# Kernel tuning notes

Measured on AMD Instinct MI355X. Metric: run time of the kernel, lower is better.

Reference implementation:

```python
import jax, jax.numpy as jnp
import numpy as np

S = 1024   # speakers_per_batch
U = 64     # utterances_per_speaker
E = 256    # model_embedding_size


def setup_inputs() -> dict:
    key = jax.random.key(0)
    k1, _ = jax.random.split(key)
    # embeds as produced by forward(): relu'd then L2-normalized rows
    raw = jax.nn.relu(jax.random.normal(k1, (S * U, E), dtype=jnp.float32))
    embeds = raw / (jnp.linalg.norm(raw, axis=1, keepdims=True) + 1e-12)
    return {
        "embeds": embeds,
        "similarity_weight": jnp.array([10.0], dtype=jnp.float32),
        "similarity_bias": jnp.array([-5.0], dtype=jnp.float32),
    }


def reference(embeds, similarity_weight, similarity_bias):
    e = embeds.reshape(S, U, E)                      # [S,U,E]
    # inclusive centroids (per speaker)
    c_incl = jnp.mean(e, axis=1)                     # [S,E]
    incl_norm = jnp.linalg.norm(c_incl, axis=1)      # [S]
    # exclusive centroids (leave-one-out per utterance)
    c_excl = (jnp.sum(e, axis=1, keepdims=True) - e) / (U - 1)  # [S,U,E]
    excl_norm = jnp.linalg.norm(c_excl, axis=2)      # [S,U]
    # off-diagonal (k != j): cosine vs inclusive centroid of speaker k
    sim = jnp.einsum('jue,ke->juk', e, c_incl) / incl_norm       # [S,U,S]
    # diagonal (k == j): cosine vs own exclusive centroid
    diag = jnp.einsum('jue,jue->ju', e, c_excl) / excl_norm      # [S,U]
    idx = jnp.arange(S)
    sim = sim.at[idx, :, idx].set(diag)
    sim = sim * similarity_weight[0] + similarity_bias[0]
    # cross-entropy against ground truth speaker ids
    logits = sim.reshape(S * U, S)                   # [SU,S]
    gt = jnp.repeat(jnp.arange(S), U)                # [SU]
    logp = jax.nn.log_softmax(logits, axis=-1)
    loss = -jnp.mean(jnp.take_along_axis(logp, gt[:, None], axis=1))
    preds = jnp.argmax(logits, axis=1)
    accuracy = jnp.mean((preds == gt).astype(jnp.float32))
    return loss, accuracy
```

## Files before the change

kernel.cpp:

```cpp
#include <hip/hip_runtime.h>
#include <math.h>

#define NS 1024
#define NU 64
#define NE 256

typedef __attribute__((ext_vector_type(4))) float f32x4;
typedef long i64x2 __attribute__((ext_vector_type(2)));

__device__ static inline unsigned int pk4_fp8(float a, float b, float c,
                                              float d) {
  int r = 0;
  r = __builtin_amdgcn_cvt_pk_fp8_f32(a, b, r, false);
  r = __builtin_amdgcn_cvt_pk_fp8_f32(c, d, r, true);
  return (unsigned int)r;
}


__global__ __launch_bounds__(256) void centroid_kernel(
    const float* __restrict__ embeds, unsigned int* __restrict__ Cb,
    unsigned long long* __restrict__ Ab, float* __restrict__ normsum,
    float* __restrict__ ssumG, unsigned int* __restrict__ pmaxG,
    float* __restrict__ out) {
  int k = blockIdx.x;
  int t = threadIdx.x;
  if (t < 64) {
    ssumG[k * 64 + t] = 0.f;
    pmaxG[k * 64 + t] = 0u;
  }
  int wave = t >> 6, e4 = t & 63;

  const float4* base =
      (const float4*)(embeds + (size_t)k * NU * NE) + wave * 16 * 64 + e4;
  float4 s = {0.f, 0.f, 0.f, 0.f};
#pragma unroll
  for (int i = 0; i < 16; ++i) {
    float4 v = base[i * 64];
    s.x += v.x; s.y += v.y; s.z += v.z; s.w += v.w;
  }
  __shared__ float4 ps[4][64];
  ps[wave][e4] = s;
  __syncthreads();
  if (t < 64) {
    float4 a = ps[0][t], b = ps[1][t], c = ps[2][t], d = ps[3][t];
    float4 s4;
    s4.x = a.x + b.x + c.x + d.x;
    s4.y = a.y + b.y + c.y + d.y;
    s4.z = a.z + b.z + c.z + d.z;
    s4.w = a.w + b.w + c.w + d.w;
    float sq = s4.x * s4.x + s4.y * s4.y + s4.z * s4.z + s4.w * s4.w;
#pragma unroll
    for (int off = 32; off; off >>= 1) sq += __shfl_xor(sq, off, 64);
    float nrm = sqrtf(sq);
    float inv = 1.f / nrm;
    unsigned int v = pk4_fp8(s4.x * inv, s4.y * inv, s4.z * inv, s4.w * inv);
    int lane_ = (((t >> 1) & 3) * 16 + (k & 15));
    int idx = (k >> 4) * 1024 + (t >> 4) * 256 + lane_ * 4 +
              (((t >> 3) & 1) << 1) + (t & 1);
    Cb[idx] = v;
    if (t == 0) {
      normsum[k] = nrm;
      if (k == 0) { out[0] = 0.f; out[1] = 0.f; }
    }
  }

  {
    int tile = t >> 6;
    int l = t & 63;
    int m = l & 15, qq = l >> 4;
    const float* rowp = embeds + (size_t)(k * 64 + tile * 16 + m) * NE;
    i64x2* Ab2 = (i64x2*)Ab;
    size_t base2 = ((size_t)k * 4 + tile) * 256 + l;
#pragma unroll
    for (int s2 = 0; s2 < 4; ++s2) {
      unsigned long long u[2];
#pragma unroll
      for (int half = 0; half < 2; ++half) {
        int sI = 2 * s2 + half;
        int k0 = sI * 32 + qq * 8;
        float4 x = *(const float4*)(rowp + k0);
        float4 y = *(const float4*)(rowp + k0 + 4);
        unsigned int lo = pk4_fp8(x.x, x.y, x.z, x.w);
        unsigned int hi = pk4_fp8(y.x, y.y, y.z, y.w);
        u[half] = ((unsigned long long)hi << 32) | lo;
      }
      i64x2 v;
      v.x = (long)u[0];
      v.y = (long)u[1];
      Ab2[base2 + s2 * 64] = v;
    }
  }
}

__global__ __launch_bounds__(256, 4) void main_kernel(
    const long* __restrict__ Ab, const long* __restrict__ Cb,
    const float* __restrict__ normsum, const float* __restrict__ wp,
    const float* __restrict__ bp, float* __restrict__ ssumG,
    unsigned int* __restrict__ pmaxG, float* __restrict__ pdiagG) {
  int t = threadIdx.x;
  int wave = t >> 6, lane = t & 63;
  int c = lane & 15, q = lane >> 4;
  int b = blockIdx.x;
  int rg = b >> 1;
  int h = b & 1;
  int jspk = rg * 2 + (wave >> 1);
  int r0 = rg * 128 + wave * 32;

  float w = *wp, bia = *bp;
  const float L2E = 1.4426950408889634f;
  float M0 = fabsf(w) + bia;
  float wl = w * L2E;
  float cl = (bia - M0) * L2E;
  float ns = normsum[jspk];

  const i64x2* Av = (const i64x2*)Ab;
  const i64x2* Bv = (const i64x2*)Cb;

  long af[2][8];
#pragma unroll
  for (int mt = 0; mt < 2; ++mt) {
    int ab2 = ((r0 >> 4) + mt) * 256 + lane;
#pragma unroll
    for (int s2 = 0; s2 < 4; ++s2) {
      i64x2 v = Av[ab2 + s2 * 64];
      af[mt][2 * s2] = v.x;
      af[mt][2 * s2 + 1] = v.y;
    }
  }

  float ssum[2][4];
  float pm[2][4];
#pragma unroll
  for (int mt = 0; mt < 2; ++mt)
#pragma unroll
    for (int r = 0; r < 4; ++r) {
      ssum[mt][r] = 0.f;
      pm[mt][r] = 0.f;
    }

  auto prefetch = [&](i64x2 (&BF)[4], int Tt) {
    int cb = (h * 32 + Tt) * 256 + lane;
#pragma unroll
    for (int s2 = 0; s2 < 4; ++s2) BF[s2] = Bv[cb + s2 * 64];
  };

  auto tile = [&](f32x4 (&ACC)[2], const i64x2 (&BF)[4]) {
    ACC[0] = (f32x4){0.f, 0.f, 0.f, 0.f};
    ACC[1] = (f32x4){0.f, 0.f, 0.f, 0.f};
    __builtin_amdgcn_s_setprio(1);
#pragma unroll
    for (int s2 = 0; s2 < 4; ++s2) {
      ACC[0] = __builtin_amdgcn_mfma_f32_16x16x32_fp8_fp8(af[0][2 * s2],
                                                          BF[s2].x, ACC[0], 0, 0, 0);
      ACC[1] = __builtin_amdgcn_mfma_f32_16x16x32_fp8_fp8(af[1][2 * s2],
                                                          BF[s2].x, ACC[1], 0, 0, 0);
      ACC[0] = __builtin_amdgcn_mfma_f32_16x16x32_fp8_fp8(af[0][2 * s2 + 1],
                                                          BF[s2].y, ACC[0], 0, 0, 0);
      ACC[1] = __builtin_amdgcn_mfma_f32_16x16x32_fp8_fp8(af[1][2 * s2 + 1],
                                                          BF[s2].y, ACC[1], 0, 0, 0);
    }
    __builtin_amdgcn_s_setprio(0);
  };

  auto epilogue = [&](f32x4 (&ACC)[2], int Tt) {
    int gt = h * 32 + Tt;
    bool diagstep = ((jspk >> 4) == gt);
#pragma unroll
    for (int mt = 0; mt < 2; ++mt) {
      f32x4 a = ACC[mt];
      if (diagstep && c == (jspk & 15)) {
#pragma unroll
        for (int r = 0; r < 4; ++r) {
          float Sv = a[r] * ns;
          float den = fmaxf(fmaf(ns, ns, 1.f) - 2.f * Sv, 1e-30f);
          float val = (Sv - 1.f) * __frsqrt_rn(den);
          float pd = exp2f(fmaf(val, wl, cl));
          pdiagG[r0 + mt * 16 + q * 4 + r] = pd;
          a[r] = val;
        }
      }
#pragma unroll
      for (int r = 0; r < 4; ++r) {
        float p = exp2f(fmaf(a[r], wl, cl));
        ssum[mt][r] += p;
        pm[mt][r] = fmaxf(pm[mt][r], p);
      }
    }
  };

  i64x2 bf0[4], bf1[4];
  f32x4 accA[2], accB[2];
  prefetch(bf0, 0);
  prefetch(bf1, 1);
  tile(accA, bf0);
#pragma unroll 1
  for (int T = 1; T < 31; T += 2) {
    prefetch(bf0, T + 1);
    tile(accB, bf1);
    epilogue(accA, T - 1);
    prefetch(bf1, T + 2);
    tile(accA, bf0);
    epilogue(accB, T);
  }
  tile(accB, bf1);
  epilogue(accA, 30);
  epilogue(accB, 31);

#pragma unroll
  for (int mt = 0; mt < 2; ++mt)
#pragma unroll
    for (int r = 0; r < 4; ++r) {
      float s = ssum[mt][r];
      s += __shfl_xor(s, 1, 64);
      s += __shfl_xor(s, 2, 64);
      s += __shfl_xor(s, 4, 64);
      s += __shfl_xor(s, 8, 64);
      float m = pm[mt][r];
      m = fmaxf(m, __shfl_xor(m, 1, 64));
      m = fmaxf(m, __shfl_xor(m, 2, 64));
      m = fmaxf(m, __shfl_xor(m, 4, 64));
      m = fmaxf(m, __shfl_xor(m, 8, 64));
      if (c == 0) {
        int row = r0 + mt * 16 + q * 4 + r;
        atomicAdd(&ssumG[row], s);
        atomicMax(&pmaxG[row], __float_as_uint(m));
      }
    }
}

__global__ __launch_bounds__(256) void reduce_kernel(
    const float* __restrict__ ssumG, const unsigned int* __restrict__ pmaxG,
    const float* __restrict__ pdiagG, float* __restrict__ out) {
  int i = blockIdx.x * 256 + threadIdx.x;
  float pd = pdiagG[i];
  float lossr = __logf(ssumG[i] / pd);
  float corr = (pd >= __uint_as_float(pmaxG[i])) ? 1.f : 0.f;
#pragma unroll
  for (int off = 32; off; off >>= 1) {
    lossr += __shfl_xor(lossr, off, 64);
    corr += __shfl_xor(corr, off, 64);
  }
  __shared__ float pl[4], pc[4];
  int wave = threadIdx.x >> 6, lane = threadIdx.x & 63;
  if (lane == 0) { pl[wave] = lossr; pc[wave] = corr; }
  __syncthreads();
  if (threadIdx.x == 0) {
    const float inv = 1.f / (float)(NS * NU);
    atomicAdd(&out[0], (pl[0] + pl[1] + pl[2] + pl[3]) * inv);
    atomicAdd(&out[1], (pc[0] + pc[1] + pc[2] + pc[3]) * inv);
  }
}

extern "C" void kernel_launch(void* const* d_in, const int* in_sizes, int n_in,
                              void* d_out, int out_size, void* d_ws,
                              size_t ws_size, hipStream_t stream) {
  const float* embeds = (const float*)d_in[0];
  const float* w = (const float*)d_in[1];
  const float* b = (const float*)d_in[2];
  float* out = (float*)d_out;
  char* ws = (char*)d_ws;
  unsigned int* Cb = (unsigned int*)ws;
  unsigned int* pmaxG = (unsigned int*)(ws + (256 << 10));
  float* ssumG = (float*)(ws + (512 << 10));
  float* pdiagG = (float*)(ws + (768 << 10));
  float* normsum = (float*)(ws + (1024 << 10));
  unsigned long long* Ab =
      (unsigned long long*)(ws + (1056 << 10));

  centroid_kernel<<<NS, 256, 0, stream>>>(embeds, Cb, Ab, normsum, ssumG,
                                          pmaxG, out);
  main_kernel<<<1024, 256, 0, stream>>>((const long*)Ab, (const long*)Cb,
                                        normsum, w, b, ssumG, pmaxG, pdiagG);
  reduce_kernel<<<NS * NU / 256, 256, 0, stream>>>(ssumG, pmaxG, pdiagG, out);
}
```

Before: 145.1 us.

## Halve per-wave row tile and split K across two accumulators to double grid

Each wave now handles 16 rows instead of 32, with the 256-deep K reduction split into two independent MFMA accumulator chains that are summed in the epilogue. The grid doubles to 2048 blocks and launch bounds target 8 blocks per SM to raise occupancy. The aim is better latency hiding and lower register pressure. The cost is that every B tile is now loaded twice as often per output row, doubling centroid traffic, and more atomics are issued.

```diff
diff --git a/kernel.cpp b/kernel.cpp
--- a/kernel.cpp
+++ b/kernel.cpp
@@ -92,7 +92,7 @@
   }
 }
 
-__global__ __launch_bounds__(256, 4) void main_kernel(
+__global__ __launch_bounds__(256, 8) void main_kernel(
     const long* __restrict__ Ab, const long* __restrict__ Cb,
     const float* __restrict__ normsum, const float* __restrict__ wp,
     const float* __restrict__ bp, float* __restrict__ ssumG,
@@ -103,8 +103,8 @@
   int b = blockIdx.x;
   int rg = b >> 1;
   int h = b & 1;
-  int jspk = rg * 2 + (wave >> 1);
-  int r0 = rg * 128 + wave * 32;
+  int jspk = rg;
+  int r0 = rg * 64 + wave * 16;
 
   float w = *wp, bia = *bp;
   const float L2E = 1.4426950408889634f;
@@ -116,27 +116,23 @@
   const i64x2* Av = (const i64x2*)Ab;
   const i64x2* Bv = (const i64x2*)Cb;
 
-  long af[2][8];
-#pragma unroll
-  for (int mt = 0; mt < 2; ++mt) {
-    int ab2 = ((r0 >> 4) + mt) * 256 + lane;
+  long af[8];
+  {
+    int ab2 = (rg * 4 + wave) * 256 + lane;
 #pragma unroll
     for (int s2 = 0; s2 < 4; ++s2) {
       i64x2 v = Av[ab2 + s2 * 64];
-      af[mt][2 * s2] = v.x;
-      af[mt][2 * s2 + 1] = v.y;
-    }
-  }
-
-  float ssum[2][4];
-  float pm[2][4];
-#pragma unroll
-  for (int mt = 0; mt < 2; ++mt)
-#pragma unroll
-    for (int r = 0; r < 4; ++r) {
-      ssum[mt][r] = 0.f;
-      pm[mt][r] = 0.f;
-    }
+      af[2 * s2] = v.x;
+      af[2 * s2 + 1] = v.y;
+    }
+  }
+
+  float ssum[4], pm[4];
+#pragma unroll
+  for (int r = 0; r < 4; ++r) {
+    ssum[r] = 0.f;
+    pm[r] = 0.f;
+  }
 
   auto prefetch = [&](i64x2 (&BF)[4], int Tt) {
     int cb = (h * 32 + Tt) * 256 + lane;
@@ -149,15 +145,15 @@
     ACC[1] = (f32x4){0.f, 0.f, 0.f, 0.f};
     __builtin_amdgcn_s_setprio(1);
 #pragma unroll
-    for (int s2 = 0; s2 < 4; ++s2) {
-      ACC[0] = __builtin_amdgcn_mfma_f32_16x16x32_fp8_fp8(af[0][2 * s2],
-                                                          BF[s2].x, ACC[0], 0, 0, 0);
-      ACC[1] = __builtin_amdgcn_mfma_f32_16x16x32_fp8_fp8(af[1][2 * s2],
-                                                          BF[s2].x, ACC[1], 0, 0, 0);
-      ACC[0] = __builtin_amdgcn_mfma_f32_16x16x32_fp8_fp8(af[0][2 * s2 + 1],
-                                                          BF[s2].y, ACC[0], 0, 0, 0);
-      ACC[1] = __builtin_amdgcn_mfma_f32_16x16x32_fp8_fp8(af[1][2 * s2 + 1],
-                                                          BF[s2].y, ACC[1], 0, 0, 0);
+    for (int s2 = 0; s2 < 2; ++s2) {
+      ACC[0] = __builtin_amdgcn_mfma_f32_16x16x32_fp8_fp8(
+          af[2 * s2], BF[s2].x, ACC[0], 0, 0, 0);
+      ACC[1] = __builtin_amdgcn_mfma_f32_16x16x32_fp8_fp8(
+          af[2 * s2 + 4], BF[s2 + 2].x, ACC[1], 0, 0, 0);
+      ACC[0] = __builtin_amdgcn_mfma_f32_16x16x32_fp8_fp8(
+          af[2 * s2 + 1], BF[s2].y, ACC[0], 0, 0, 0);
+      ACC[1] = __builtin_amdgcn_mfma_f32_16x16x32_fp8_fp8(
+          af[2 * s2 + 5], BF[s2 + 2].y, ACC[1], 0, 0, 0);
     }
     __builtin_amdgcn_s_setprio(0);
   };
@@ -165,26 +161,23 @@
   auto epilogue = [&](f32x4 (&ACC)[2], int Tt) {
     int gt = h * 32 + Tt;
     bool diagstep = ((jspk >> 4) == gt);
-#pragma unroll
-    for (int mt = 0; mt < 2; ++mt) {
-      f32x4 a = ACC[mt];
-      if (diagstep && c == (jspk & 15)) {
-#pragma unroll
-        for (int r = 0; r < 4; ++r) {
-          float Sv = a[r] * ns;
-          float den = fmaxf(fmaf(ns, ns, 1.f) - 2.f * Sv, 1e-30f);
-          float val = (Sv - 1.f) * __frsqrt_rn(den);
-          float pd = exp2f(fmaf(val, wl, cl));
-          pdiagG[r0 + mt * 16 + q * 4 + r] = pd;
-          a[r] = val;
-        }
+    f32x4 a = ACC[0] + ACC[1];
+    if (diagstep && c == (jspk & 15)) {
+#pragma unroll
+      for (int r = 0; r < 4; ++r) {
+        float Sv = a[r] * ns;
+        float den = fmaxf(fmaf(ns, ns, 1.f) - 2.f * Sv, 1e-30f);
+        float val = (Sv - 1.f) * __frsqrt_rn(den);
+        float pd = exp2f(fmaf(val, wl, cl));
+        pdiagG[r0 + q * 4 + r] = pd;
+        a[r] = val;
       }
-#pragma unroll
-      for (int r = 0; r < 4; ++r) {
-        float p = exp2f(fmaf(a[r], wl, cl));
-        ssum[mt][r] += p;
-        pm[mt][r] = fmaxf(pm[mt][r], p);
-      }
+    }
+#pragma unroll
+    for (int r = 0; r < 4; ++r) {
+      float p = exp2f(fmaf(a[r], wl, cl));
+      ssum[r] += p;
+      pm[r] = fmaxf(pm[r], p);
     }
   };
 
@@ -207,25 +200,23 @@
   epilogue(accB, 31);
 
 #pragma unroll
-  for (int mt = 0; mt < 2; ++mt)
-#pragma unroll
-    for (int r = 0; r < 4; ++r) {
-      float s = ssum[mt][r];
-      s += __shfl_xor(s, 1, 64);
-      s += __shfl_xor(s, 2, 64);
-      s += __shfl_xor(s, 4, 64);
-      s += __shfl_xor(s, 8, 64);
-      float m = pm[mt][r];
-      m = fmaxf(m, __shfl_xor(m, 1, 64));
-      m = fmaxf(m, __shfl_xor(m, 2, 64));
-      m = fmaxf(m, __shfl_xor(m, 4, 64));
-      m = fmaxf(m, __shfl_xor(m, 8, 64));
-      if (c == 0) {
-        int row = r0 + mt * 16 + q * 4 + r;
-        atomicAdd(&ssumG[row], s);
-        atomicMax(&pmaxG[row], __float_as_uint(m));
-      }
-    }
+  for (int r = 0; r < 4; ++r) {
+    float s = ssum[r];
+    s += __shfl_xor(s, 1, 64);
+    s += __shfl_xor(s, 2, 64);
+    s += __shfl_xor(s, 4, 64);
+    s += __shfl_xor(s, 8, 64);
+    float m = pm[r];
+    m = fmaxf(m, __shfl_xor(m, 1, 64));
+    m = fmaxf(m, __shfl_xor(m, 2, 64));
+    m = fmaxf(m, __shfl_xor(m, 4, 64));
+    m = fmaxf(m, __shfl_xor(m, 8, 64));
+    if (c == 0) {
+      int row = r0 + q * 4 + r;
+      atomicAdd(&ssumG[row], s);
+      atomicMax(&pmaxG[row], __float_as_uint(m));
+    }
+  }
 }
 
 __global__ __launch_bounds__(256) void reduce_kernel(
@@ -269,7 +260,7 @@
 
   centroid_kernel<<<NS, 256, 0, stream>>>(embeds, Cb, Ab, normsum, ssumG,
                                           pmaxG, out);
-  main_kernel<<<1024, 256, 0, stream>>>((const long*)Ab, (const long*)Cb,
+  main_kernel<<<2048, 256, 0, stream>>>((const long*)Ab, (const long*)Cb,
                                         normsum, w, b, ssumG, pmaxG, pdiagG);
   reduce_kernel<<<NS * NU / 256, 256, 0, stream>>>(ssumG, pmaxG, pdiagG, out);
 }
```

New measurement: 378.9 us. 2.61x slower.

## Stage shared centroid tiles through LDS with async global-to-LDS loads

Applied to the files above, without the earlier changes.

Every wave in a block previously loaded the same fp8 centroid tile from global memory into its own registers. Now the four waves load the tile once into a double-buffered LDS array using global_load_lds, then each wave reads it from LDS. The hand-interleaved two-accumulator pipeline, which overlapped MFMA of one tile with the exp epilogue of the previous one, is replaced by a simple loop with a __syncthreads per tile. The occupancy hint in launch_bounds is also dropped. This trades redundant global/L2 traffic for barrier stalls and less overlap between matrix math and the epilogue.

```diff
diff --git a/kernel.cpp b/kernel.cpp
--- a/kernel.cpp
+++ b/kernel.cpp
@@ -14,6 +14,12 @@
   r = __builtin_amdgcn_cvt_pk_fp8_f32(a, b, r, false);
   r = __builtin_amdgcn_cvt_pk_fp8_f32(c, d, r, true);
   return (unsigned int)r;
+}
+
+__device__ static inline void gload_lds16(const void* gsrc, void* ldst) {
+  __builtin_amdgcn_global_load_lds(
+      (const __attribute__((address_space(1))) unsigned int*)gsrc,
+      (__attribute__((address_space(3))) unsigned int*)ldst, 16, 0, 0);
 }
 
 
@@ -92,7 +98,7 @@
   }
 }
 
-__global__ __launch_bounds__(256, 4) void main_kernel(
+__global__ __launch_bounds__(256) void main_kernel(
     const long* __restrict__ Ab, const long* __restrict__ Cb,
     const float* __restrict__ normsum, const float* __restrict__ wp,
     const float* __restrict__ bp, float* __restrict__ ssumG,
@@ -116,6 +122,13 @@
   const i64x2* Av = (const i64x2*)Ab;
   const i64x2* Bv = (const i64x2*)Cb;
 
+  __shared__ i64x2 ldsB[2][256];
+
+  auto stage = [&](int buf, int Tt) {
+    const i64x2* src = Bv + ((h * 32 + Tt) * 256 + wave * 64 + lane);
+    gload_lds16((const void*)src, (void*)&ldsB[buf][wave * 64]);
+  };
+
   long af[2][8];
 #pragma unroll
   for (int mt = 0; mt < 2; ++mt) {
@@ -128,8 +141,7 @@
     }
   }
 
-  float ssum[2][4];
-  float pm[2][4];
+  float ssum[2][4], pm[2][4];
 #pragma unroll
   for (int mt = 0; mt < 2; ++mt)
 #pragma unroll
@@ -138,36 +150,39 @@
       pm[mt][r] = 0.f;
     }
 
-  auto prefetch = [&](i64x2 (&BF)[4], int Tt) {
-    int cb = (h * 32 + Tt) * 256 + lane;
-#pragma unroll
-    for (int s2 = 0; s2 < 4; ++s2) BF[s2] = Bv[cb + s2 * 64];
-  };
-
-  auto tile = [&](f32x4 (&ACC)[2], const i64x2 (&BF)[4]) {
-    ACC[0] = (f32x4){0.f, 0.f, 0.f, 0.f};
-    ACC[1] = (f32x4){0.f, 0.f, 0.f, 0.f};
+  stage(0, 0);
+  __syncthreads();
+
+#pragma unroll 1
+  for (int T = 0; T < 32; ++T) {
+    int cur = T & 1;
+    if (T + 1 < 32) stage(cur ^ 1, T + 1);
+
+    i64x2 bf[4];
+#pragma unroll
+    for (int s2 = 0; s2 < 4; ++s2) bf[s2] = ldsB[cur][s2 * 64 + lane];
+
+    f32x4 a0 = {0.f, 0.f, 0.f, 0.f};
+    f32x4 a1 = {0.f, 0.f, 0.f, 0.f};
     __builtin_amdgcn_s_setprio(1);
 #pragma unroll
     for (int s2 = 0; s2 < 4; ++s2) {
-      ACC[0] = __builtin_amdgcn_mfma_f32_16x16x32_fp8_fp8(af[0][2 * s2],
-                                                          BF[s2].x, ACC[0], 0, 0, 0);
-      ACC[1] = __builtin_amdgcn_mfma_f32_16x16x32_fp8_fp8(af[1][2 * s2],
-                                                          BF[s2].x, ACC[1], 0, 0, 0);
-      ACC[0] = __builtin_amdgcn_mfma_f32_16x16x32_fp8_fp8(af[0][2 * s2 + 1],
-                                                          BF[s2].y, ACC[0], 0, 0, 0);
-      ACC[1] = __builtin_amdgcn_mfma_f32_16x16x32_fp8_fp8(af[1][2 * s2 + 1],
-                                                          BF[s2].y, ACC[1], 0, 0, 0);
+      a0 = __builtin_amdgcn_mfma_f32_16x16x32_fp8_fp8(af[0][2 * s2], bf[s2].x,
+                                                      a0, 0, 0, 0);
+      a1 = __builtin_amdgcn_mfma_f32_16x16x32_fp8_fp8(af[1][2 * s2], bf[s2].x,
+                                                      a1, 0, 0, 0);
+      a0 = __builtin_amdgcn_mfma_f32_16x16x32_fp8_fp8(af[0][2 * s2 + 1],
+                                                      bf[s2].y, a0, 0, 0, 0);
+      a1 = __builtin_amdgcn_mfma_f32_16x16x32_fp8_fp8(af[1][2 * s2 + 1],
+                                                      bf[s2].y, a1, 0, 0, 0);
     }
     __builtin_amdgcn_s_setprio(0);
-  };
-
-  auto epilogue = [&](f32x4 (&ACC)[2], int Tt) {
-    int gt = h * 32 + Tt;
+
+    int gt = h * 32 + T;
     bool diagstep = ((jspk >> 4) == gt);
 #pragma unroll
     for (int mt = 0; mt < 2; ++mt) {
-      f32x4 a = ACC[mt];
+      f32x4 a = (mt == 0) ? a0 : a1;
       if (diagstep && c == (jspk & 15)) {
 #pragma unroll
         for (int r = 0; r < 4; ++r) {
@@ -186,25 +201,9 @@
         pm[mt][r] = fmaxf(pm[mt][r], p);
       }
     }
-  };
-
-  i64x2 bf0[4], bf1[4];
-  f32x4 accA[2], accB[2];
-  prefetch(bf0, 0);
-  prefetch(bf1, 1);
-  tile(accA, bf0);
-#pragma unroll 1
-  for (int T = 1; T < 31; T += 2) {
-    prefetch(bf0, T + 1);
-    tile(accB, bf1);
-    epilogue(accA, T - 1);
-    prefetch(bf1, T + 2);
-    tile(accA, bf0);
-    epilogue(accB, T);
-  }
-  tile(accB, bf1);
-  epilogue(accA, 30);
-  epilogue(accB, 31);
+
+    __syncthreads();
+  }
 
 #pragma unroll
   for (int mt = 0; mt < 2; ++mt)
```

Result: slower. 152.2 us (+4.9%).

## Give each wave a full speaker's 64 rows to double B-fragment reuse

Applied to the files above, without the earlier changes.

Each wave now handles one whole speaker (four 16-row M tiles) instead of 32 rows, so every loaded centroid fragment feeds twice as many MFMAs. The grid is halved to 512 blocks. The launch-bounds occupancy hint and the setprio calls are dropped, and exp2f is replaced with the hardware exp2 builtin. This cuts centroid reloads and instruction overhead per output, but it raises register pressure and reduces parallelism, which may lower occupancy and latency hiding.

```diff
diff --git a/kernel.cpp b/kernel.cpp
--- a/kernel.cpp
+++ b/kernel.cpp
@@ -92,7 +92,7 @@
   }
 }
 
-__global__ __launch_bounds__(256, 4) void main_kernel(
+__global__ __launch_bounds__(256) void main_kernel(
     const long* __restrict__ Ab, const long* __restrict__ Cb,
     const float* __restrict__ normsum, const float* __restrict__ wp,
     const float* __restrict__ bp, float* __restrict__ ssumG,
@@ -103,8 +103,8 @@
   int b = blockIdx.x;
   int rg = b >> 1;
   int h = b & 1;
-  int jspk = rg * 2 + (wave >> 1);
-  int r0 = rg * 128 + wave * 32;
+  int jspk = rg * 4 + wave;
+  int r0 = jspk * 64;
 
   float w = *wp, bia = *bp;
   const float L2E = 1.4426950408889634f;
@@ -116,9 +116,9 @@
   const i64x2* Av = (const i64x2*)Ab;
   const i64x2* Bv = (const i64x2*)Cb;
 
-  long af[2][8];
-#pragma unroll
-  for (int mt = 0; mt < 2; ++mt) {
+  long af[4][8];
+#pragma unroll
+  for (int mt = 0; mt < 4; ++mt) {
     int ab2 = ((r0 >> 4) + mt) * 256 + lane;
 #pragma unroll
     for (int s2 = 0; s2 < 4; ++s2) {
@@ -128,10 +128,10 @@
     }
   }
 
-  float ssum[2][4];
-  float pm[2][4];
-#pragma unroll
-  for (int mt = 0; mt < 2; ++mt)
+  float ssum[4][4];
+  float pm[4][4];
+#pragma unroll
+  for (int mt = 0; mt < 4; ++mt)
 #pragma unroll
     for (int r = 0; r < 4; ++r) {
       ssum[mt][r] = 0.f;
@@ -144,29 +144,27 @@
     for (int s2 = 0; s2 < 4; ++s2) BF[s2] = Bv[cb + s2 * 64];
   };
 
-  auto tile = [&](f32x4 (&ACC)[2], const i64x2 (&BF)[4]) {
-    ACC[0] = (f32x4){0.f, 0.f, 0.f, 0.f};
-    ACC[1] = (f32x4){0.f, 0.f, 0.f, 0.f};
-    __builtin_amdgcn_s_setprio(1);
+  auto tile = [&](f32x4 (&ACC)[4], const i64x2 (&BF)[4]) {
+#pragma unroll
+    for (int mt = 0; mt < 4; ++mt) ACC[mt] = (f32x4){0.f, 0.f, 0.f, 0.f};
 #pragma unroll
     for (int s2 = 0; s2 < 4; ++s2) {
-      ACC[0] = __builtin_amdgcn_mfma_f32_16x16x32_fp8_fp8(af[0][2 * s2],
-                                                          BF[s2].x, ACC[0], 0, 0, 0);
-      ACC[1] = __builtin_amdgcn_mfma_f32_16x16x32_fp8_fp8(af[1][2 * s2],
-                                                          BF[s2].x, ACC[1], 0, 0, 0);
-      ACC[0] = __builtin_amdgcn_mfma_f32_16x16x32_fp8_fp8(af[0][2 * s2 + 1],
-                                                          BF[s2].y, ACC[0], 0, 0, 0);
-      ACC[1] = __builtin_amdgcn_mfma_f32_16x16x32_fp8_fp8(af[1][2 * s2 + 1],
-                                                          BF[s2].y, ACC[1], 0, 0, 0);
-    }
-    __builtin_amdgcn_s_setprio(0);
+#pragma unroll
+      for (int mt = 0; mt < 4; ++mt)
+        ACC[mt] = __builtin_amdgcn_mfma_f32_16x16x32_fp8_fp8(
+            af[mt][2 * s2], BF[s2].x, ACC[mt], 0, 0, 0);
+#pragma unroll
+      for (int mt = 0; mt < 4; ++mt)
+        ACC[mt] = __builtin_amdgcn_mfma_f32_16x16x32_fp8_fp8(
+            af[mt][2 * s2 + 1], BF[s2].y, ACC[mt], 0, 0, 0);
+    }
   };
 
-  auto epilogue = [&](f32x4 (&ACC)[2], int Tt) {
+  auto epilogue = [&](f32x4 (&ACC)[4], int Tt) {
     int gt = h * 32 + Tt;
     bool diagstep = ((jspk >> 4) == gt);
 #pragma unroll
-    for (int mt = 0; mt < 2; ++mt) {
+    for (int mt = 0; mt < 4; ++mt) {
       f32x4 a = ACC[mt];
       if (diagstep && c == (jspk & 15)) {
 #pragma unroll
@@ -174,14 +172,14 @@
           float Sv = a[r] * ns;
           float den = fmaxf(fmaf(ns, ns, 1.f) - 2.f * Sv, 1e-30f);
           float val = (Sv - 1.f) * __frsqrt_rn(den);
-          float pd = exp2f(fmaf(val, wl, cl));
+          float pd = __builtin_amdgcn_exp2f(fmaf(val, wl, cl));
           pdiagG[r0 + mt * 16 + q * 4 + r] = pd;
           a[r] = val;
         }
       }
 #pragma unroll
       for (int r = 0; r < 4; ++r) {
-        float p = exp2f(fmaf(a[r], wl, cl));
+        float p = __builtin_amdgcn_exp2f(fmaf(a[r], wl, cl));
         ssum[mt][r] += p;
         pm[mt][r] = fmaxf(pm[mt][r], p);
       }
@@ -189,7 +187,7 @@
   };
 
   i64x2 bf0[4], bf1[4];
-  f32x4 accA[2], accB[2];
+  f32x4 accA[4], accB[4];
   prefetch(bf0, 0);
   prefetch(bf1, 1);
   tile(accA, bf0);
@@ -207,7 +205,7 @@
   epilogue(accB, 31);
 
 #pragma unroll
-  for (int mt = 0; mt < 2; ++mt)
+  for (int mt = 0; mt < 4; ++mt)
 #pragma unroll
     for (int r = 0; r < 4; ++r) {
       float s = ssum[mt][r];
@@ -269,7 +267,7 @@
 
   centroid_kernel<<<NS, 256, 0, stream>>>(embeds, Cb, Ab, normsum, ssumG,
                                           pmaxG, out);
-  main_kernel<<<1024, 256, 0, stream>>>((const long*)Ab, (const long*)Cb,
-                                        normsum, w, b, ssumG, pmaxG, pdiagG);
+  main_kernel<<<512, 256, 0, stream>>>((const long*)Ab, (const long*)Cb,
+                                       normsum, w, b, ssumG, pmaxG, pdiagG);
   reduce_kernel<<<NS * NU / 256, 256, 0, stream>>>(ssumG, pmaxG, pdiagG, out);
 }
```

After: 143.1 us. About the same (-1.4%).
